# Performance work log

Hardware: AMD Instinct MI355X
Metric: run time of the kernel (lower is better)

## Reference

```python
import jax, jax.numpy as jnp
import numpy as np
from jax import lax

DN = ('NCHW', 'OIHW', 'NCHW')
HIDDEN = 9      # ProposalModule(out_channels, len(scales)*len(ratios)) -> hidden_dim = 9
N_ANC = 9       # default n_anchors
C_IN = 2048
B, H, W = 32, 25, 25
N_POS = 2048
N_NEG = 2048
N_FLAT = B * H * W * N_ANC  # 180000


def setup_inputs() -> dict:
    key = jax.random.key(0)
    ks = jax.random.split(key, 10)
    feature_maps = jax.random.normal(ks[0], (B, C_IN, H, W), dtype=jnp.float32)
    pos_anc_idxs = jax.random.randint(ks[1], (N_POS,), 0, N_FLAT)
    neg_anc_idxs = jax.random.randint(ks[2], (N_NEG,), 0, N_FLAT)
    # xyxy anchor boxes in feature-map coords with strictly positive width/height
    xy = jax.random.uniform(ks[3], (N_POS, 2), dtype=jnp.float32) * 20.0
    wh = jax.random.uniform(ks[4], (N_POS, 2), dtype=jnp.float32) * 5.0 + 1.0
    pos_ancs = jnp.concatenate([xy, xy + wh], axis=1)
    # conv params (torch OIHW layout), fan-in scaled init
    Wh = jax.random.normal(ks[5], (HIDDEN, C_IN, 3, 3), dtype=jnp.float32) / np.sqrt(C_IN * 9)
    bh = jnp.zeros((HIDDEN,), dtype=jnp.float32)
    Wc = jax.random.normal(ks[6], (N_ANC, HIDDEN, 1, 1), dtype=jnp.float32) / np.sqrt(HIDDEN)
    bc = jnp.zeros((N_ANC,), dtype=jnp.float32)
    Wr = jax.random.normal(ks[7], (N_ANC * 4, HIDDEN, 1, 1), dtype=jnp.float32) / np.sqrt(HIDDEN)
    br = jnp.zeros((N_ANC * 4,), dtype=jnp.float32)
    return {'feature_maps': feature_maps, 'pos_anc_idxs': pos_anc_idxs,
            'neg_anc_idxs': neg_anc_idxs, 'pos_ancs': pos_ancs,
            'Wh': Wh, 'bh': bh, 'Wc': Wc, 'bc': bc, 'Wr': Wr, 'br': br}


def _conv(x, w, b, pad):
    y = lax.conv_general_dilated(x, w, (1, 1), pad, dimension_numbers=DN)
    return y + b[None, :, None, None]


def reference(feature_maps, pos_anc_idxs, neg_anc_idxs, pos_ancs, Wh, bh, Wc, bc, Wr, br):
    # ProposalModule train-mode forward (dropout = identity, deterministic)
    x = jax.nn.relu(_conv(feature_maps, Wh, bh, 'SAME'))          # [b, hidden, h, w]
    conf_pred = _conv(x, Wc, bc, 'VALID')                          # [b, n_anc, h, w]
    offsets_pred = _conv(x, Wr, br, 'VALID')                       # [b, 4*n_anc, h, w]

    conf_flat = jnp.transpose(conf_pred, (0, 2, 3, 1)).reshape(-1)       # [b*h*w*n_anc]
    pos_conf = conf_flat[pos_anc_idxs]
    neg_conf = conf_flat[neg_anc_idxs]
    off_flat = jnp.transpose(offsets_pred, (0, 2, 3, 1)).reshape(-1, 4)  # [b*h*w*n_anc, 4]
    pos_offsets = off_flat[pos_anc_idxs]

    # _generate_proposals: xyxy -> cxcywh, apply offsets, back to xyxy
    cx = (pos_ancs[:, 0] + pos_ancs[:, 2]) * 0.5
    cy = (pos_ancs[:, 1] + pos_ancs[:, 3]) * 0.5
    w = pos_ancs[:, 2] - pos_ancs[:, 0]
    h = pos_ancs[:, 3] - pos_ancs[:, 1]
    ncx = cx + pos_offsets[:, 0] * w
    ncy = cy + pos_offsets[:, 1] * h
    nw = w * jnp.exp(pos_offsets[:, 2])
    nh = h * jnp.exp(pos_offsets[:, 3])
    proposals = jnp.stack([ncx - nw * 0.5, ncy - nh * 0.5,
                           ncx + nw * 0.5, ncy + nh * 0.5], axis=-1)
    return pos_conf, neg_conf, pos_offsets, proposals
```

## Files before the change

### kernel.cpp

```cpp
#include <hip/hip_runtime.h>
#include <hip/hip_bf16.h>
#include <math.h>

#define C_IN   2048
#define HID    9
#define NIDX   4096
#define PLANE  (NIDX * HID)

#define NGRP   32
#define NT     16
#define NBUF   4
#define ICAP   192
#define BUFB   5440

#define BFRAG_OFF 0
#define CNT_OFF   262144
#define LIST_OFF  (CNT_OFF + 64)
#define PART_OFF  (LIST_OFF + 32 * ICAP)
#define WS_NEED   (((size_t)PART_OFF + (size_t)PLANE) * 4)

typedef short  bf16x8 __attribute__((ext_vector_type(8)));
typedef float  f32x4  __attribute__((ext_vector_type(4)));

__device__ __forceinline__ unsigned short bits_of(float v) {
  __hip_bfloat16 h = __float2bfloat16(v);
  return *reinterpret_cast<unsigned short*>(&h);
}

__global__ void prep_kernel(const float* __restrict__ Wh,
                            const int*   __restrict__ pos_idx,
                            const int*   __restrict__ neg_idx,
                            float*       __restrict__ wsf,
                            unsigned*    __restrict__ wsu) {
  int e = blockIdx.x * 256 + threadIdx.x;
  if (e < 512 * 2 * 64) {
    int lane = e & 63, s = (e >> 6) & 1, tc = e >> 7;
    int n = lane & 15, q = lane >> 4;
    unsigned short h[8];
#pragma unroll
    for (int j = 0; j < 8; j++) {
      float v = 0.f;
      if (n < 9) {
        if (s == 0) {
          int tap = 2 * q + (j >> 2), ch = j & 3;
          v = Wh[(n * C_IN + tc * 4 + ch) * 9 + tap];
        } else if (q == 0 && j < 4) {
          v = Wh[(n * C_IN + tc * 4 + j) * 9 + 8];
        }
      }
      h[j] = bits_of(v);
    }
    uint4 dv;
    dv.x = h[0] | ((unsigned)h[1] << 16);
    dv.y = h[2] | ((unsigned)h[3] << 16);
    dv.z = h[4] | ((unsigned)h[5] << 16);
    dv.w = h[6] | ((unsigned)h[7] << 16);
    ((uint4*)(wsu + BFRAG_OFF))[e] = dv;
  }
  if (e < PLANE) wsf[PART_OFF + e] = 0.f;
  if (e < NIDX) {
    int flat = (e < 2048) ? pos_idx[e] : neg_idx[e - 2048];
    int pw = flat / 9;
    int b  = pw / 625;
    int p  = pw - b * 625;
    int h  = p / 25, w = p - h * 25;
    unsigned mask = 0;
#pragma unroll
    for (int dh = 0; dh < 3; dh++)
#pragma unroll
      for (int dw = 0; dw < 3; dw++)
        if (h + dh >= 1 && h + dh <= 25 && w + dw >= 1 && w + dw <= 25)
          mask |= 1u << (dh * 3 + dw);
    unsigned pack = (unsigned)p | (mask << 10) | ((unsigned)e << 19);
    int* icnt = (int*)(wsu + CNT_OFF);
    int* bcnt = (int*)(wsu + CNT_OFF + 32);
    if (mask == 0x1FFu) {
      int n = atomicAdd(&icnt[b], 1);
      if (n < ICAP) wsu[LIST_OFF + b * ICAP + n] = pack;
    } else {
      int m = atomicAdd(&bcnt[b], 1);
      if (m < ICAP) wsu[LIST_OFF + b * ICAP + (ICAP - 1 - m)] = pack;
    }
  }
}

__global__ __launch_bounds__(256, 4) void conv_gather(
    const float* __restrict__ feat,
    const unsigned* __restrict__ wsu,
    float* __restrict__ part) {
  __shared__ __align__(16) char stage[NBUF * BUFB];
  __shared__ int slots_lds[ICAP];
  __shared__ int prod_flag[NT];
  __shared__ int cons_cnt[NT];

  const int t = threadIdx.x, g = blockIdx.x, b = blockIdx.y;
  const int lane = t & 63, wv = t >> 6;

  const int icnt = min(((const int*)(wsu + CNT_OFF))[b], ICAP);
  const int cnt  = min(icnt + ((const int*)(wsu + CNT_OFF + 32))[b], ICAP);

  if (t < NT) { prod_flag[t] = 0; cons_cnt[t] = 0; }
  if (t < ICAP) {
    int phys = (t < icnt) ? t : (ICAP - 1 - (t - icnt));
    slots_lds[t] = (int)(wsu[LIST_OFF + b * ICAP + phys] >> 19);
  }
  __syncthreads();

  const float* gbase = feat + ((size_t)b * C_IN + (size_t)g * 64) * 625;

  if (wv >= 2) {
    for (int k = wv - 2; k < NT; k += 2) {
      if (k >= NBUF)
        while (__hip_atomic_load(&cons_cnt[k - NBUF], __ATOMIC_ACQUIRE,
                                 __HIP_MEMORY_SCOPE_WORKGROUP) < 2)
          __builtin_amdgcn_s_sleep(1);
      const float* gt = gbase + (size_t)k * 2500;
      char* bufk = stage + (k & (NBUF - 1)) * BUFB;
      float v0[10], v1[10], v2[10], v3[10];
#pragma unroll
      for (int r = 0; r < 10; r++) {
        int hw = r * 64 + lane;
        bool ok = hw < 625;
        v0[r] = ok ? gt[hw]        : 0.f;
        v1[r] = ok ? gt[625 + hw]  : 0.f;
        v2[r] = ok ? gt[1250 + hw] : 0.f;
        v3[r] = ok ? gt[1875 + hw] : 0.f;
      }
#pragma unroll
      for (int r = 0; r < 10; r++) {
        int hw = r * 64 + lane;
        uint2 dv;
        dv.x = bits_of(v0[r]) | ((unsigned)bits_of(v1[r]) << 16);
        dv.y = bits_of(v2[r]) | ((unsigned)bits_of(v3[r]) << 16);
        if (hw < 625) *(uint2*)(bufk + (26 + hw) * 8) = dv;
      }
      if (lane == 0)
        __hip_atomic_store(&prod_flag[k], 1, __ATOMIC_RELEASE,
                           __HIP_MEMORY_SCOPE_WORKGROUP);
    }
    return;
  }

  const int n = lane & 15, q = lane >> 4;
  const int t0o = ((q == 0) ? -26 : (q == 1) ? -24 : (q == 2) ? 0  : 24) * 8;
  const int t1o = ((q == 0) ? -25 : (q == 1) ? -1  : (q == 2) ? 1  : 25) * 8;
  const int t8o = 26 * 8;

  const int mtbase = wv * 6;
  int pb[6]; unsigned mk[6]; int st[6];
#pragma unroll
  for (int i = 0; i < 6; i++) {
    int mt = mtbase + i;
    int e = mt * 16 + n;
    int p = 0; unsigned m = 0;
    if (e < cnt) {
      int phys = (e < icnt) ? e : (ICAP - 1 - (e - icnt));
      unsigned pack = wsu[LIST_OFF + b * ICAP + phys];
      p = (int)(pack & 1023u);
      m = (pack >> 10) & 511u;
    }
    pb[i] = (26 + p) * 8;
    mk[i] = (e < cnt) ? m : 0u;
    st[i] = (mt * 16 >= cnt) ? 0 : (((mt + 1) * 16 <= icnt) ? 1 : 2);
  }

  f32x4 acc[6];
#pragma unroll
  for (int i = 0; i < 6; i++) acc[i] = (f32x4){0.f, 0.f, 0.f, 0.f};

  const uint4* btab = (const uint4*)(wsu + BFRAG_OFF);

  for (int k = 0; k < NT; k++) {
    const int tc = g * 16 + k;
    bf16x8 bf0 = __builtin_bit_cast(bf16x8, btab[(tc * 2 + 0) * 64 + lane]);
    bf16x8 bf1 = __builtin_bit_cast(bf16x8, btab[(tc * 2 + 1) * 64 + lane]);
    while (__hip_atomic_load(&prod_flag[k], __ATOMIC_ACQUIRE,
                             __HIP_MEMORY_SCOPE_WORKGROUP) == 0)
      __builtin_amdgcn_s_sleep(1);
    const char* bufk = stage + (k & (NBUF - 1)) * BUFB;
#pragma unroll
    for (int i = 0; i < 6; i++) {
      if (st[i] == 0) continue;
      const char* ba = bufk + pb[i];
      int2 lo = *(const int2*)(ba + t0o);
      int2 hi = *(const int2*)(ba + t1o);
      int2 r8 = *(const int2*)(ba + t8o);
      if (st[i] == 2) {
        bool b0 = (mk[i] >> (2 * q)) & 1u;
        bool b1 = (mk[i] >> (2 * q + 1)) & 1u;
        bool b8 = (mk[i] >> 8) & 1u;
        lo.x = b0 ? lo.x : 0; lo.y = b0 ? lo.y : 0;
        hi.x = b1 ? hi.x : 0; hi.y = b1 ? hi.y : 0;
        r8.x = b8 ? r8.x : 0; r8.y = b8 ? r8.y : 0;
      }
      int4 a0 = {lo.x, lo.y, hi.x, hi.y};
      acc[i] = __builtin_amdgcn_mfma_f32_16x16x32_bf16(
          __builtin_bit_cast(bf16x8, a0), bf0, acc[i], 0, 0, 0);
      int4 a1 = {r8.x, r8.y, 0, 0};
      acc[i] = __builtin_amdgcn_mfma_f32_16x16x32_bf16(
          __builtin_bit_cast(bf16x8, a1), bf1, acc[i], 0, 0, 0);
    }
    if (lane == 0)
      __hip_atomic_fetch_add(&cons_cnt[k], 1, __ATOMIC_RELEASE,
                             __HIP_MEMORY_SCOPE_WORKGROUP);
  }

  if (n < 9) {
#pragma unroll
    for (int i = 0; i < 6; i++) {
      if (st[i] == 0) continue;
#pragma unroll
      for (int reg = 0; reg < 4; reg++) {
        int e = (mtbase + i) * 16 + q * 4 + reg;
        if (e < cnt) {
          int slot = slots_lds[e];
          atomicAdd(&part[slot * 9 + n], acc[i][reg]);
        }
      }
    }
  }
}

__global__ void heads_kernel(const float* __restrict__ part,
                             const int*   __restrict__ pos_idx,
                             const int*   __restrict__ neg_idx,
                             const float* __restrict__ pos_ancs,
                             const float* __restrict__ bh,
                             const float* __restrict__ Wc,
                             const float* __restrict__ bc,
                             const float* __restrict__ Wr,
                             const float* __restrict__ br,
                             float*       __restrict__ out) {
  int i = blockIdx.x * 256 + threadIdx.x;
  if (i >= NIDX) return;
  int flat = (i < 2048) ? pos_idx[i] : neg_idx[i - 2048];
  int anc = flat % 9;
  const float* pp = part + (size_t)i * 9;
  float xr[9];
#pragma unroll
  for (int j = 0; j < 9; j++) {
    float v = bh[j] + pp[j];
    xr[j] = v > 0.f ? v : 0.f;
  }
  float conf = bc[anc];
#pragma unroll
  for (int j = 0; j < 9; j++) conf += xr[j] * Wc[anc * 9 + j];
  out[i] = conf;
  if (i < 2048) {
    float off[4];
#pragma unroll
    for (int k = 0; k < 4; k++) {
      float sacc = br[anc * 4 + k];
#pragma unroll
      for (int j = 0; j < 9; j++) sacc += xr[j] * Wr[(anc * 4 + k) * 9 + j];
      off[k] = sacc;
      out[4096 + i * 4 + k] = sacc;
    }
    float x1 = pos_ancs[i * 4 + 0], y1 = pos_ancs[i * 4 + 1];
    float x2 = pos_ancs[i * 4 + 2], y2 = pos_ancs[i * 4 + 3];
    float cx = (x1 + x2) * 0.5f, cy = (y1 + y2) * 0.5f;
    float w = x2 - x1, h = y2 - y1;
    float ncx = cx + off[0] * w, ncy = cy + off[1] * h;
    float nw = w * expf(off[2]), nh = h * expf(off[3]);
    out[12288 + i * 4 + 0] = ncx - nw * 0.5f;
    out[12288 + i * 4 + 1] = ncy - nh * 0.5f;
    out[12288 + i * 4 + 2] = ncx + nw * 0.5f;
    out[12288 + i * 4 + 3] = ncy + nh * 0.5f;
  }
}

extern "C" void kernel_launch(void* const* d_in, const int* in_sizes, int n_in,
                              void* d_out, int out_size, void* d_ws, size_t ws_size,
                              hipStream_t stream) {
  const float* feat     = (const float*)d_in[0];
  const int*   pos_idx  = (const int*)d_in[1];
  const int*   neg_idx  = (const int*)d_in[2];
  const float* pos_ancs = (const float*)d_in[3];
  const float* Wh       = (const float*)d_in[4];
  const float* bh       = (const float*)d_in[5];
  const float* Wc       = (const float*)d_in[6];
  const float* bc       = (const float*)d_in[7];
  const float* Wr       = (const float*)d_in[8];
  const float* br       = (const float*)d_in[9];
  float* out = (float*)d_out;

  float*    wsf  = (float*)d_ws;
  unsigned* wsu  = (unsigned*)d_ws;
  float*    part = wsf + PART_OFF;

  hipMemsetAsync((char*)d_ws + (size_t)CNT_OFF * 4, 0, 64 * 4, stream);
  prep_kernel<<<256, 256, 0, stream>>>(Wh, pos_idx, neg_idx, wsf, wsu);
  conv_gather<<<dim3(NGRP, 32), 256, 0, stream>>>(feat, wsu, part);
  heads_kernel<<<16, 256, 0, stream>>>(part, pos_idx, neg_idx, pos_ancs,
                                       bh, Wc, bc, Wr, br, out);
}
```

Measured before the change: 267.6 us.

## Fuse weight packing and index bucketing into the conv gather kernel

Removes the separate prep kernel: each conv block now scans all 4096 indices to build its own batch's anchor list in LDS, and loads and converts its 64-channel weight slice into an LDS table. The consumer waves then assemble MFMA B fragments from LDS instead of reading a prepacked global table. This removes one launch and a global round trip, but adds redundant index scanning and weight conversion in every one of 1024 blocks, plus extra LDS use that may lower occupancy.

```diff
diff --git a/kernel.cpp b/kernel.cpp
--- a/kernel.cpp
+++ b/kernel.cpp
@@ -12,12 +12,9 @@
 #define NBUF   4
 #define ICAP   192
 #define BUFB   5440
-
-#define BFRAG_OFF 0
-#define CNT_OFF   262144
-#define LIST_OFF  (CNT_OFF + 64)
-#define PART_OFF  (LIST_OFF + 32 * ICAP)
-#define WS_NEED   (((size_t)PART_OFF + (size_t)PLANE) * 4)
+#define WROW   10
+
+#define WS_NEED ((size_t)PLANE * 4)
 
 typedef short  bf16x8 __attribute__((ext_vector_type(8)));
 typedef float  f32x4  __attribute__((ext_vector_type(4)));
@@ -27,83 +24,24 @@
   return *reinterpret_cast<unsigned short*>(&h);
 }
 
-__global__ void prep_kernel(const float* __restrict__ Wh,
-                            const int*   __restrict__ pos_idx,
-                            const int*   __restrict__ neg_idx,
-                            float*       __restrict__ wsf,
-                            unsigned*    __restrict__ wsu) {
-  int e = blockIdx.x * 256 + threadIdx.x;
-  if (e < 512 * 2 * 64) {
-    int lane = e & 63, s = (e >> 6) & 1, tc = e >> 7;
-    int n = lane & 15, q = lane >> 4;
-    unsigned short h[8];
-#pragma unroll
-    for (int j = 0; j < 8; j++) {
-      float v = 0.f;
-      if (n < 9) {
-        if (s == 0) {
-          int tap = 2 * q + (j >> 2), ch = j & 3;
-          v = Wh[(n * C_IN + tc * 4 + ch) * 9 + tap];
-        } else if (q == 0 && j < 4) {
-          v = Wh[(n * C_IN + tc * 4 + j) * 9 + 8];
-        }
-      }
-      h[j] = bits_of(v);
-    }
-    uint4 dv;
-    dv.x = h[0] | ((unsigned)h[1] << 16);
-    dv.y = h[2] | ((unsigned)h[3] << 16);
-    dv.z = h[4] | ((unsigned)h[5] << 16);
-    dv.w = h[6] | ((unsigned)h[7] << 16);
-    ((uint4*)(wsu + BFRAG_OFF))[e] = dv;
-  }
-  if (e < PLANE) wsf[PART_OFF + e] = 0.f;
-  if (e < NIDX) {
-    int flat = (e < 2048) ? pos_idx[e] : neg_idx[e - 2048];
-    int pw = flat / 9;
-    int b  = pw / 625;
-    int p  = pw - b * 625;
-    int h  = p / 25, w = p - h * 25;
-    unsigned mask = 0;
-#pragma unroll
-    for (int dh = 0; dh < 3; dh++)
-#pragma unroll
-      for (int dw = 0; dw < 3; dw++)
-        if (h + dh >= 1 && h + dh <= 25 && w + dw >= 1 && w + dw <= 25)
-          mask |= 1u << (dh * 3 + dw);
-    unsigned pack = (unsigned)p | (mask << 10) | ((unsigned)e << 19);
-    int* icnt = (int*)(wsu + CNT_OFF);
-    int* bcnt = (int*)(wsu + CNT_OFF + 32);
-    if (mask == 0x1FFu) {
-      int n = atomicAdd(&icnt[b], 1);
-      if (n < ICAP) wsu[LIST_OFF + b * ICAP + n] = pack;
-    } else {
-      int m = atomicAdd(&bcnt[b], 1);
-      if (m < ICAP) wsu[LIST_OFF + b * ICAP + (ICAP - 1 - m)] = pack;
-    }
-  }
-}
-
 __global__ __launch_bounds__(256, 4) void conv_gather(
     const float* __restrict__ feat,
-    const unsigned* __restrict__ wsu,
+    const float* __restrict__ Wh,
+    const int*   __restrict__ pos_idx,
+    const int*   __restrict__ neg_idx,
     float* __restrict__ part) {
   __shared__ __align__(16) char stage[NBUF * BUFB];
-  __shared__ int slots_lds[ICAP];
+  __shared__ unsigned pack_lds[ICAP];
+  __shared__ unsigned short w_lds[64 * 9 * WROW];
   __shared__ int prod_flag[NT];
   __shared__ int cons_cnt[NT];
+  __shared__ int lcnt_i, lcnt_b, bld_done;
 
   const int t = threadIdx.x, g = blockIdx.x, b = blockIdx.y;
   const int lane = t & 63, wv = t >> 6;
 
-  const int icnt = min(((const int*)(wsu + CNT_OFF))[b], ICAP);
-  const int cnt  = min(icnt + ((const int*)(wsu + CNT_OFF + 32))[b], ICAP);
-
   if (t < NT) { prod_flag[t] = 0; cons_cnt[t] = 0; }
-  if (t < ICAP) {
-    int phys = (t < icnt) ? t : (ICAP - 1 - (t - icnt));
-    slots_lds[t] = (int)(wsu[LIST_OFF + b * ICAP + phys] >> 19);
-  }
+  if (t == 0) { lcnt_i = 0; lcnt_b = 0; bld_done = 0; }
   __syncthreads();
 
   const float* gbase = feat + ((size_t)b * C_IN + (size_t)g * 64) * 625;
@@ -141,6 +79,46 @@
     return;
   }
 
+  for (int e = t; e < NIDX; e += 128) {
+    int flat = (e < 2048) ? pos_idx[e] : neg_idx[e - 2048];
+    int pw = flat / 9;
+    int bb = pw / 625;
+    if (bb != b) continue;
+    int p = pw - bb * 625;
+    int h = p / 25, w = p - h * 25;
+    unsigned mask = 0;
+#pragma unroll
+    for (int dh = 0; dh < 3; dh++)
+#pragma unroll
+      for (int dw = 0; dw < 3; dw++)
+        if (h + dh >= 1 && h + dh <= 25 && w + dw >= 1 && w + dw <= 25)
+          mask |= 1u << (dh * 3 + dw);
+    unsigned pack = (unsigned)p | (mask << 10) | ((unsigned)e << 19);
+    if (mask == 0x1FFu) {
+      int pos = atomicAdd(&lcnt_i, 1);
+      if (pos < ICAP) pack_lds[pos] = pack;
+    } else {
+      int m = atomicAdd(&lcnt_b, 1);
+      if (m < ICAP) pack_lds[ICAP - 1 - m] = pack;
+    }
+  }
+  for (int m = t; m < 9 * 576; m += 128) {
+    int n = m / 576, r = m - n * 576;
+    float v = Wh[((size_t)n * C_IN + (size_t)g * 64) * 9 + r];
+    w_lds[r * WROW + n] = bits_of(v);
+  }
+  if (lane == 0)
+    __hip_atomic_fetch_add(&bld_done, 1, __ATOMIC_RELEASE,
+                           __HIP_MEMORY_SCOPE_WORKGROUP);
+  while (__hip_atomic_load(&bld_done, __ATOMIC_ACQUIRE,
+                           __HIP_MEMORY_SCOPE_WORKGROUP) < 2)
+    __builtin_amdgcn_s_sleep(1);
+
+  const int icnt = min(__hip_atomic_load(&lcnt_i, __ATOMIC_RELAXED,
+                                         __HIP_MEMORY_SCOPE_WORKGROUP), ICAP);
+  const int cnt  = min(icnt + __hip_atomic_load(&lcnt_b, __ATOMIC_RELAXED,
+                                         __HIP_MEMORY_SCOPE_WORKGROUP), ICAP);
+
   const int n = lane & 15, q = lane >> 4;
   const int t0o = ((q == 0) ? -26 : (q == 1) ? -24 : (q == 2) ? 0  : 24) * 8;
   const int t1o = ((q == 0) ? -25 : (q == 1) ? -1  : (q == 2) ? 1  : 25) * 8;
@@ -155,7 +133,7 @@
     int p = 0; unsigned m = 0;
     if (e < cnt) {
       int phys = (e < icnt) ? e : (ICAP - 1 - (e - icnt));
-      unsigned pack = wsu[LIST_OFF + b * ICAP + phys];
+      unsigned pack = pack_lds[phys];
       p = (int)(pack & 1023u);
       m = (pack >> 10) & 511u;
     }
@@ -168,12 +146,20 @@
 #pragma unroll
   for (int i = 0; i < 6; i++) acc[i] = (f32x4){0.f, 0.f, 0.f, 0.f};
 
-  const uint4* btab = (const uint4*)(wsu + BFRAG_OFF);
-
   for (int k = 0; k < NT; k++) {
-    const int tc = g * 16 + k;
-    bf16x8 bf0 = __builtin_bit_cast(bf16x8, btab[(tc * 2 + 0) * 64 + lane]);
-    bf16x8 bf1 = __builtin_bit_cast(bf16x8, btab[(tc * 2 + 1) * 64 + lane]);
+    bf16x8 bf0, bf1;
+#pragma unroll
+    for (int j = 0; j < 8; j++) {
+      int cl = k * 4 + (j & 3);
+      int tap = 2 * q + (j >> 2);
+      bf0[j] = (n < 9) ? (short)w_lds[(cl * 9 + tap) * WROW + n] : (short)0;
+    }
+#pragma unroll
+    for (int j = 0; j < 8; j++) {
+      bf1[j] = (q == 0 && j < 4 && n < 9)
+                   ? (short)w_lds[((k * 4 + j) * 9 + 8) * WROW + n]
+                   : (short)0;
+    }
     while (__hip_atomic_load(&prod_flag[k], __ATOMIC_ACQUIRE,
                              __HIP_MEMORY_SCOPE_WORKGROUP) == 0)
       __builtin_amdgcn_s_sleep(1);
@@ -213,7 +199,8 @@
       for (int reg = 0; reg < 4; reg++) {
         int e = (mtbase + i) * 16 + q * 4 + reg;
         if (e < cnt) {
-          int slot = slots_lds[e];
+          int phys = (e < icnt) ? e : (ICAP - 1 - (e - icnt));
+          int slot = (int)(pack_lds[phys] >> 19);
           atomicAdd(&part[slot * 9 + n], acc[i][reg]);
         }
       }
@@ -284,13 +271,11 @@
   const float* br       = (const float*)d_in[9];
   float* out = (float*)d_out;
 
-  float*    wsf  = (float*)d_ws;
-  unsigned* wsu  = (unsigned*)d_ws;
-  float*    part = wsf + PART_OFF;
-
-  hipMemsetAsync((char*)d_ws + (size_t)CNT_OFF * 4, 0, 64 * 4, stream);
-  prep_kernel<<<256, 256, 0, stream>>>(Wh, pos_idx, neg_idx, wsf, wsu);
-  conv_gather<<<dim3(NGRP, 32), 256, 0, stream>>>(feat, wsu, part);
+  float* part = (float*)d_ws;
+
+  hipMemsetAsync(d_ws, 0, WS_NEED, stream);
+  conv_gather<<<dim3(NGRP, 32), 256, 0, stream>>>(
+      feat, Wh, pos_idx, neg_idx, part);
   heads_kernel<<<16, 256, 0, stream>>>(part, pos_idx, neg_idx, pos_ancs,
                                        bh, Wc, bc, Wr, br, out);
 }
```

After: 274.7 us. +2.6%, slower.
